# Optimization experiments

Hardware: AMD Instinct MI355X
Metric: run time of the kernel (lower is better)

Reference implementation:

```python
import jax, jax.numpy as jnp
import numpy as np

B, T, F, H = 1024, 512, 40, 50


def setup_inputs() -> dict:
    key = jax.random.key(0)
    ks = jax.random.split(key, 9)
    s = 0.1
    return {
        "x": jax.random.normal(ks[0], (B, T, F), dtype=jnp.float32),
        "W_ih": jax.random.normal(ks[1], (4 * H, F), dtype=jnp.float32) * s,
        "W_hh": jax.random.normal(ks[2], (4 * H, H), dtype=jnp.float32) * s,
        "b_ih": jax.random.normal(ks[3], (4 * H,), dtype=jnp.float32) * s,
        "b_hh": jax.random.normal(ks[4], (4 * H,), dtype=jnp.float32) * s,
        "W1": jax.random.normal(ks[5], (10, H), dtype=jnp.float32) * s,
        "b1": jax.random.normal(ks[6], (10,), dtype=jnp.float32) * s,
        "W2": jax.random.normal(ks[7], (1, 10), dtype=jnp.float32) * s,
        "b2": jax.random.normal(ks[8], (1,), dtype=jnp.float32) * s,
    }


def reference(x, W_ih, W_hh, b_ih, b_hh, W1, b1, W2, b2):
    b, t, f = x.shape
    h = W_hh.shape[1]
    # Precompute input projections for all timesteps: [T, B, 4H]
    xg = jnp.einsum("btf,gf->tbg", x, W_ih) + (b_ih + b_hh)

    h0 = jnp.zeros((b, h), dtype=x.dtype)
    c0 = jnp.zeros((b, h), dtype=x.dtype).at[:, 0].set(1.0)

    def step(carry, xg_t):
        hx, cx = carry
        gates = xg_t + hx @ W_hh.T  # [B, 4H]
        i, fg, g, o = jnp.split(gates, 4, axis=-1)  # PyTorch gate order i,f,g,o
        i = jax.nn.sigmoid(i)
        fg = jax.nn.sigmoid(fg)
        g = jnp.tanh(g)
        o = jax.nn.sigmoid(o)
        cx = fg * cx + i * g
        hx = o * jnp.tanh(cx)
        return (hx, cx), None

    (hx, _), _ = jax.lax.scan(step, (h0, c0), xg)
    head = jax.nn.relu(hx @ W1.T + b1) @ W2.T + b2  # [B, 1]
    return head + x[:, -1, 0:1]
```

## Files before the change

kernel.cpp:

```cpp
#include <hip/hip_runtime.h>


constexpr int kT   = 512;
constexpr int kF   = 40;
constexpr int kH   = 50;
constexpr int kMB  = 2;
constexpr int kRowS = 104;
constexpr int kGRow = 208;

typedef __attribute__((ext_vector_type(8))) short bf16x8;
typedef __attribute__((ext_vector_type(4))) float f32x4;

__device__ __forceinline__ unsigned short f2bf(float f) {
    union { float f; unsigned u; } v; v.f = f;
    return (unsigned short)((v.u + 0x7FFFu + ((v.u >> 16) & 1u)) >> 16);
}
__device__ __forceinline__ float fast_sigmoid(float v) {
    return __builtin_amdgcn_rcpf(1.f + __expf(-v));
}
__device__ __forceinline__ float fast_tanh(float v) {
    return 1.f - 2.f * __builtin_amdgcn_rcpf(__expf(2.f * v) + 1.f);
}

__global__ __launch_bounds__(256, 2)
void lstm_mfma_2cu(
    const float* __restrict__ x,
    const float* __restrict__ W_ih,
    const float* __restrict__ W_hh,
    const float* __restrict__ b_ih,
    const float* __restrict__ b_hh,
    const float* __restrict__ W1,
    const float* __restrict__ b1,
    const float* __restrict__ W2,
    const float* __restrict__ b2,
    float* __restrict__ out)
{
    const int tid  = threadIdx.x;
    const int lane = tid & 63;
    const int wave = tid >> 6;
    const int bb   = blockIdx.x;
    const int m16  = lane & 15;
    const int q    = lane >> 4;

    __shared__ short sh_comb[2][16][kRowS];
    __shared__ float sh_g[kMB][kGRow];
    __shared__ float sh_hf[kMB][kH + 2];
    __shared__ float sh_head[kMB][10];

    const int t0 = (wave == 3) ? 9 : wave * 3;
    const int NT = (wave == 3) ? 4 : 3;

    { int* z = (int*)sh_comb; for (int i = tid; i < 1664; i += 256) z[i] = 0; }

    bf16x8 wa[4][3];
    float  bias[4][4];
    const int uA = m16 >> 2, gA = m16 & 3;
#pragma unroll
    for (int i = 0; i < 4; ++i) {
        const int tl = t0 + i;
        const int unitA = 4 * tl + uA;
        const bool live = (i < NT) && (unitA < kH);
        const int orow = live ? (unitA + 50 * gA) : 0;
#pragma unroll
        for (int kk = 0; kk < 3; ++kk) {
            bf16x8 v;
#pragma unroll
            for (int j = 0; j < 8; ++j) {
                const int k = kk * 32 + q * 8 + j;
                float wv = 0.f;
                if (live) {
                    if (k < kF)           wv = W_ih[orow * kF + k];
                    else if (k < kF + kH) wv = W_hh[orow * kH + (k - kF)];
                }
                v[j] = (short)f2bf(wv);
            }
            wa[i][kk] = v;
        }
        const int uD = 4 * tl + q;
#pragma unroll
        for (int r = 0; r < 4; ++r)
            bias[i][r] = (i < NT && uD < kH)
                       ? (b_ih[uD + 50 * r] + b_hh[uD + 50 * r]) : 0.f;
    }

    const bool pw = (tid < kMB * kH);
    const int  pm = pw ? (tid / kH) : 0;
    const int  pu = pw ? (tid % kH) : 0;
    float c     = (pw && pu == 0) ? 1.f : 0.f;
    float lasth = 0.f;

    const bool xs = (tid >= 128 && tid < 128 + kMB * 20);
    const int  xi = xs ? (tid - 128) : 0;
    const int  xm = xi / 20, xd = xi % 20;
    const float* xrow = x + ((size_t)(bb * kMB + xm) * kT) * kF + 2 * xd;

    float2 pa = {0.f, 0.f}, pb = {0.f, 0.f};
    __syncthreads();
    if (xs) {
        float2 v0 = *(const float2*)xrow;
        unsigned pk = (unsigned)f2bf(v0.x) | ((unsigned)f2bf(v0.y) << 16);
        *(unsigned*)&sh_comb[0][xm][2 * xd] = pk;
        pa = *(const float2*)(xrow + (size_t)1 * kF);
        pb = *(const float2*)(xrow + (size_t)2 * kF);
    }
    __syncthreads();

    auto step = [&](int t, int CUR, float2& pf) {
        const short* rowp = &sh_comb[CUR][m16][0];
        bf16x8 bv0 = *(const bf16x8*)(rowp +      q * 8);
        bf16x8 bv1 = *(const bf16x8*)(rowp + 32 + q * 8);
        bf16x8 bv2 = *(const bf16x8*)(rowp + 64 + q * 8);
#pragma unroll
        for (int i = 0; i < 4; ++i) {
            if (i < NT) {
                f32x4 d;
                d[0] = bias[i][0]; d[1] = bias[i][1];
                d[2] = bias[i][2]; d[3] = bias[i][3];
                d = __builtin_amdgcn_mfma_f32_16x16x32_bf16(wa[i][0], bv0, d, 0, 0, 0);
                d = __builtin_amdgcn_mfma_f32_16x16x32_bf16(wa[i][1], bv1, d, 0, 0, 0);
                d = __builtin_amdgcn_mfma_f32_16x16x32_bf16(wa[i][2], bv2, d, 0, 0, 0);
                if (m16 < kMB)
                    *(f32x4*)&sh_g[m16][16 * (t0 + i) + 4 * q] = d;
            }
        }
        __syncthreads();

        short* nbuf = &sh_comb[CUR ^ 1][0][0];
        if (pw) {
            f32x4 g = *(const f32x4*)&sh_g[pm][4 * pu];
            float i_s = fast_sigmoid(g[0]);
            float f_s = fast_sigmoid(g[1]);
            float g_t = fast_tanh   (g[2]);
            float o_s = fast_sigmoid(g[3]);
            c = fmaf(f_s, c, i_s * g_t);
            lasth = o_s * fast_tanh(c);
            if (t + 1 < kT)
                nbuf[pm * kRowS + kF + pu] = (short)f2bf(lasth);
        } else if (xs) {
            if (t + 1 < kT) {
                unsigned pk = (unsigned)f2bf(pf.x) | ((unsigned)f2bf(pf.y) << 16);
                *(unsigned*)&nbuf[xm * kRowS + 2 * xd] = pk;
            }
            if (t + 3 < kT)
                pf = *(const float2*)(xrow + (size_t)(t + 3) * kF);
        }
        __syncthreads();
    };

    for (int t = 0; t < kT; t += 2) {
        step(t,     0, pa);
        step(t + 1, 1, pb);
    }

    if (pw) sh_hf[pm][pu] = lasth;
    __syncthreads();
    if (tid < kMB * 10) {
        const int m = tid / 10, j = tid % 10;
        float acc = b1[j];
#pragma unroll
        for (int k = 0; k < kH; ++k) acc = fmaf(sh_hf[m][k], W1[j * kH + k], acc);
        sh_head[m][j] = fmaxf(acc, 0.f);
    }
    __syncthreads();
    if (tid < kMB) {
        float acc = b2[0];
#pragma unroll
        for (int j2 = 0; j2 < 10; ++j2) acc = fmaf(sh_head[tid][j2], W2[j2], acc);
        const int bidx = bb * kMB + tid;
        out[bidx] = acc + x[((size_t)bidx * kT + (kT - 1)) * kF];
    }
}

extern "C" void kernel_launch(void* const* d_in, const int* in_sizes, int n_in,
                              void* d_out, int out_size, void* d_ws, size_t ws_size,
                              hipStream_t stream) {
    const float* x    = (const float*)d_in[0];
    const float* W_ih = (const float*)d_in[1];
    const float* W_hh = (const float*)d_in[2];
    const float* b_ih = (const float*)d_in[3];
    const float* b_hh = (const float*)d_in[4];
    const float* W1   = (const float*)d_in[5];
    const float* b1   = (const float*)d_in[6];
    const float* W2   = (const float*)d_in[7];
    const float* b2   = (const float*)d_in[8];
    float* out = (float*)d_out;

    lstm_mfma_2cu<<<dim3(1024 / kMB), dim3(256), 0, stream>>>(
        x, W_ih, W_hh, b_ih, b_hh, W1, b1, W2, b2, out);
}
```

Baseline: 358.3 us.

## Fuse gate activation into owning wave to drop one barrier per step

Each wave now applies the LSTM pointwise cell update to the gate tiles it computed itself. The results go through a wave-private shared buffer instead of a block-wide gate array, which removes one __syncthreads per timestep. The x-prefetch work is spread across lanes 32-41 of every wave instead of a dedicated thread range. The cost is an intra-wave LDS round trip that relies on implicit wave-level ordering, plus remapped hidden-state ownership.

```diff
diff --git a/kernel.cpp b/kernel.cpp
--- a/kernel.cpp
+++ b/kernel.cpp
@@ -1,12 +1,11 @@
 #include <hip/hip_runtime.h>
 
 
-constexpr int kT   = 512;
-constexpr int kF   = 40;
-constexpr int kH   = 50;
-constexpr int kMB  = 2;
+constexpr int kT    = 512;
+constexpr int kF    = 40;
+constexpr int kH    = 50;
+constexpr int kMB   = 2;
 constexpr int kRowS = 104;
-constexpr int kGRow = 208;
 
 typedef __attribute__((ext_vector_type(8))) short bf16x8;
 typedef __attribute__((ext_vector_type(4))) float f32x4;
@@ -23,7 +22,7 @@
 }
 
 __global__ __launch_bounds__(256, 2)
-void lstm_mfma_2cu(
+void lstm_mfma_fused(
     const float* __restrict__ x,
     const float* __restrict__ W_ih,
     const float* __restrict__ W_hh,
@@ -42,8 +41,8 @@
     const int m16  = lane & 15;
     const int q    = lane >> 4;
 
-    __shared__ short sh_comb[2][16][kRowS];
-    __shared__ float sh_g[kMB][kGRow];
+    __shared__ __align__(16) short sh_comb[2][16][kRowS];
+    __shared__ __align__(16) float sh_wg[4][32][4];
     __shared__ float sh_hf[kMB][kH + 2];
     __shared__ float sh_head[kMB][10];
 
@@ -53,7 +52,7 @@
     { int* z = (int*)sh_comb; for (int i = tid; i < 1664; i += 256) z[i] = 0; }
 
     bf16x8 wa[4][3];
-    float  bias[4][4];
+    f32x4  bias4[4];
     const int uA = m16 >> 2, gA = m16 & 3;
 #pragma unroll
     for (int i = 0; i < 4; ++i) {
@@ -79,24 +78,26 @@
         const int uD = 4 * tl + q;
 #pragma unroll
         for (int r = 0; r < 4; ++r)
-            bias[i][r] = (i < NT && uD < kH)
-                       ? (b_ih[uD + 50 * r] + b_hh[uD + 50 * r]) : 0.f;
+            bias4[i][r] = (i < NT && uD < kH)
+                        ? (b_ih[uD + 50 * r] + b_hh[uD + 50 * r]) : 0.f;
     }
 
-    const bool pw = (tid < kMB * kH);
-    const int  pm = pw ? (tid / kH) : 0;
-    const int  pu = pw ? (tid % kH) : 0;
-    float c     = (pw && pu == 0) ? 1.f : 0.f;
-    float lasth = 0.f;
+    const int oi = lane >> 3;
+    const int om = (lane >> 2) & 1;
+    const int oq = lane & 3;
+    const int ou = 4 * (t0 + oi) + oq;
+    const bool ow = (lane < 32) && (oi < NT) && (ou < kH);
+    float c    = (ow && ou == 0) ? 1.f : 0.f;
+    float hreg = 0.f;
 
-    const bool xs = (tid >= 128 && tid < 128 + kMB * 20);
-    const int  xi = xs ? (tid - 128) : 0;
-    const int  xm = xi / 20, xd = xi % 20;
+    const bool xst = (lane >= 32 && lane < 42);
+    const int  fid = xst ? (wave * 10 + (lane - 32)) : 0;
+    const int  xm = fid / 20, xd = fid % 20;
     const float* xrow = x + ((size_t)(bb * kMB + xm) * kT) * kF + 2 * xd;
 
     float2 pa = {0.f, 0.f}, pb = {0.f, 0.f};
     __syncthreads();
-    if (xs) {
+    if (xst) {
         float2 v0 = *(const float2*)xrow;
         unsigned pk = (unsigned)f2bf(v0.x) | ((unsigned)f2bf(v0.y) << 16);
         *(unsigned*)&sh_comb[0][xm][2 * xd] = pk;
@@ -113,36 +114,33 @@
 #pragma unroll
         for (int i = 0; i < 4; ++i) {
             if (i < NT) {
-                f32x4 d;
-                d[0] = bias[i][0]; d[1] = bias[i][1];
-                d[2] = bias[i][2]; d[3] = bias[i][3];
+                f32x4 d = bias4[i];
                 d = __builtin_amdgcn_mfma_f32_16x16x32_bf16(wa[i][0], bv0, d, 0, 0, 0);
                 d = __builtin_amdgcn_mfma_f32_16x16x32_bf16(wa[i][1], bv1, d, 0, 0, 0);
                 d = __builtin_amdgcn_mfma_f32_16x16x32_bf16(wa[i][2], bv2, d, 0, 0, 0);
                 if (m16 < kMB)
-                    *(f32x4*)&sh_g[m16][16 * (t0 + i) + 4 * q] = d;
+                    *(f32x4*)&sh_wg[wave][8 * i + 4 * m16 + q][0] = d;
             }
         }
-        __syncthreads();
-
         short* nbuf = &sh_comb[CUR ^ 1][0][0];
-        if (pw) {
-            f32x4 g = *(const f32x4*)&sh_g[pm][4 * pu];
-            float i_s = fast_sigmoid(g[0]);
-            float f_s = fast_sigmoid(g[1]);
-            float g_t = fast_tanh   (g[2]);
-            float o_s = fast_sigmoid(g[3]);
-            c = fmaf(f_s, c, i_s * g_t);
-            lasth = o_s * fast_tanh(c);
-            if (t + 1 < kT)
-                nbuf[pm * kRowS + kF + pu] = (short)f2bf(lasth);
-        } else if (xs) {
+        if (xst) {
             if (t + 1 < kT) {
                 unsigned pk = (unsigned)f2bf(pf.x) | ((unsigned)f2bf(pf.y) << 16);
                 *(unsigned*)&nbuf[xm * kRowS + 2 * xd] = pk;
             }
             if (t + 3 < kT)
                 pf = *(const float2*)(xrow + (size_t)(t + 3) * kF);
+        }
+        if (ow) {
+            f32x4 g = *(const f32x4*)&sh_wg[wave][lane][0];
+            float i_s = fast_sigmoid(g[0]);
+            float f_s = fast_sigmoid(g[1]);
+            float g_t = fast_tanh   (g[2]);
+            float o_s = fast_sigmoid(g[3]);
+            c = fmaf(f_s, c, i_s * g_t);
+            hreg = o_s * fast_tanh(c);
+            if (t + 1 < kT)
+                nbuf[om * kRowS + kF + ou] = (short)f2bf(hreg);
         }
         __syncthreads();
     };
@@ -152,7 +150,7 @@
         step(t + 1, 1, pb);
     }
 
-    if (pw) sh_hf[pm][pu] = lasth;
+    if (ow) sh_hf[om][ou] = hreg;
     __syncthreads();
     if (tid < kMB * 10) {
         const int m = tid / 10, j = tid % 10;
@@ -185,6 +183,6 @@
     const float* b2   = (const float*)d_in[8];
     float* out = (float*)d_out;
 
-    lstm_mfma_2cu<<<dim3(1024 / kMB), dim3(256), 0, stream>>>(
+    lstm_mfma_fused<<<dim3(1024 / kMB), dim3(256), 0, stream>>>(
         x, W_ih, W_hh, b_ih, b_hh, W1, b1, W2, b2, out);
 }
```

Result: slower. 370.1 us (+3.3%).
